# Kernel tuning notes

Measured on AMD Instinct MI355X. Metric: run time of the kernel, lower is better.

Reference implementation:

```python
import jax, jax.numpy as jnp
import numpy as np

EPS = 1e-8        # slot-attention epsilon
LN_EPS = 1e-5     # torch LayerNorm default
NUM_ITERS = 3

def _ln(x, g, b):
    m = jnp.mean(x, axis=-1, keepdims=True)
    v = jnp.var(x, axis=-1, keepdims=True)
    return (x - m) * jax.lax.rsqrt(v + LN_EPS) * g + b

def setup_inputs() -> dict:
    key = jax.random.key(0)
    ks = jax.random.split(key, 24)
    B, N, D, S, K, H = 64, 4096, 256, 256, 8, 512
    sc = 0.02
    return {
        "inputs": jax.random.normal(ks[0], (B, N, D), dtype=jnp.float32),
        "noise": jax.random.normal(ks[1], (B, K, S), dtype=jnp.float32),
        "slot_mu": jax.random.normal(ks[2], (1, 1, S)) * sc,
        "slot_log_sigma": jax.random.normal(ks[3], (1, 1, S)) * sc,
        "g_in": jnp.ones((D,)), "b_in": jnp.zeros((D,)),
        "g_sl": jnp.ones((S,)), "b_sl": jnp.zeros((S,)),
        "g_mlp": jnp.ones((S,)), "b_mlp": jnp.zeros((S,)),
        "Wq": jax.random.normal(ks[4], (S, S)) * sc,
        "Wk": jax.random.normal(ks[5], (S, D)) * sc,
        "Wv": jax.random.normal(ks[6], (S, D)) * sc,
        "W_ih": jax.random.normal(ks[7], (3 * S, S)) * sc,
        "W_hh": jax.random.normal(ks[8], (3 * S, S)) * sc,
        "b_ih": jnp.zeros((3 * S,)), "b_hh": jnp.zeros((3 * S,)),
        "W1": jax.random.normal(ks[9], (H, S)) * sc,
        "b1": jnp.zeros((H,)),
        "W2": jax.random.normal(ks[10], (S, H)) * sc,
        "b2": jnp.zeros((S,)),
    }

def _gru_cell(x, h, W_ih, W_hh, b_ih, b_hh):
    gi = x @ W_ih.T + b_ih
    gh = h @ W_hh.T + b_hh
    ir, iz, inn = jnp.split(gi, 3, axis=-1)
    hr, hz, hn = jnp.split(gh, 3, axis=-1)
    r = jax.nn.sigmoid(ir + hr)
    z = jax.nn.sigmoid(iz + hz)
    n = jnp.tanh(inn + r * hn)
    return (1.0 - z) * n + z * h

def reference(inputs, noise, slot_mu, slot_log_sigma, g_in, b_in, g_sl, b_sl,
              g_mlp, b_mlp, Wq, Wk, Wv, W_ih, W_hh, b_ih, b_hh, W1, b1, W2, b2):
    S = Wq.shape[0]
    slots = slot_mu + jnp.exp(slot_log_sigma) * noise          # [B,K,S]
    x = _ln(inputs, g_in, b_in)                                # [B,N,D]
    k = (x @ Wk.T) * (S ** -0.5)                               # [B,N,S]
    v = x @ Wv.T                                               # [B,N,S]
    for i in range(NUM_ITERS):
        slots_prev = slots
        q = _ln(slots, g_sl, b_sl) @ Wq.T                      # [B,K,S]
        attn_logits = jnp.einsum('bns,bks->bnk', k, q)         # [B,N,K]
        attn = jax.nn.softmax(attn_logits, axis=-1) + EPS      # softmax over slots
        attn = attn / jnp.sum(attn, axis=1, keepdims=True)     # normalize over inputs
        updates = jnp.einsum('bnk,bns->bks', attn, v)          # [B,K,S]
        slots = _gru_cell(updates, slots_prev, W_ih, W_hh, b_ih, b_hh)
        if i < NUM_ITERS - 1:
            h = jax.nn.relu(_ln(slots, g_mlp, b_mlp) @ W1.T + b1)
            slots = slots + (h @ W2.T + b2)
    return slots
```

## Files before the change

kernel.cpp:

```cpp
#include <hip/hip_runtime.h>
#include <math.h>

#define NB 64
#define NN 4096
#define ND 256
#define NS 256
#define NK 8
#define NH 512
#define NROW (NB*NN)
#define NSLOT (NB*NK)
#define EPSA 1e-8f

typedef unsigned short u16;
typedef unsigned int   u32;
typedef __bf16 bf16x8 __attribute__((ext_vector_type(8)));
typedef float  f32x4  __attribute__((ext_vector_type(4)));

__device__ __forceinline__ float bf2f(u16 u) {
  union { u32 i; float f; } v; v.i = ((u32)u) << 16; return v.f;
}
__device__ __forceinline__ u16 f2bf(float f) {
  union { float f; u32 i; } v; v.f = f;
  u32 x = v.i;
  return (u16)((x + 0x7FFFu + ((x >> 16) & 1u)) >> 16);
}

#define OFF_KV     0ULL
#define OFF_SLOTS  268435456ULL
#define OFF_QBF    268959744ULL
#define OFF_UPDP   269221888ULL
#define OFF_SUMSP  277610496ULL
#define OFF_WC     277643264ULL
#define OFF_WQT    277905408ULL
#define OFF_WIHT   278167552ULL
#define OFF_WHHT   278953984ULL
#define OFF_W1T    279740416ULL
#define OFF_W2T    280264704ULL

__global__ __launch_bounds__(256) void prep_kernel(
    const float* __restrict__ Wq, const float* __restrict__ Wk, const float* __restrict__ Wv,
    const float* __restrict__ Wih, const float* __restrict__ Whh,
    const float* __restrict__ W1, const float* __restrict__ W2,
    u16* __restrict__ Wc, float* __restrict__ WqT, float* __restrict__ WihT,
    float* __restrict__ WhhT, float* __restrict__ W1T, float* __restrict__ W2T)
{
  int idx = blockIdx.x * 256 + threadIdx.x;
  if (idx < 512*256) {
    int j = idx >> 8, d = idx & 255;
    float w = (j < 256) ? Wk[idx] * 0.0625f : Wv[idx - 65536];
    Wc[idx] = f2bf(w);
    W1T[d*512 + j] = W1[idx];
  }
  if (idx < 256*256) {
    int j = idx >> 8, d = idx & 255;
    WqT[d*256 + j] = Wq[idx];
  }
  if (idx < 768*256) {
    int j = idx >> 8, d = idx & 255;
    WihT[d*768 + j] = Wih[idx];
    WhhT[d*768 + j] = Whh[idx];
  }
  if (idx < 256*512) {
    int j = idx >> 9, h = idx & 511;
    W2T[h*256 + j] = W2[idx];
  }
}

__global__ __launch_bounds__(256) void slots_init_kernel(
    const float* __restrict__ noise, const float* __restrict__ mu,
    const float* __restrict__ lsig, float* __restrict__ slots)
{
  int idx = blockIdx.x * 256 + threadIdx.x;
  int s = idx & 255;
  slots[idx] = mu[s] + expf(lsig[s]) * noise[idx];
}

__global__ __launch_bounds__(256) void lngemm_kernel(
    const float* __restrict__ x, const float* __restrict__ gw, const float* __restrict__ bw,
    const u16* __restrict__ Wc, u16* __restrict__ kv)
{
  __shared__ u16 As[16384];
  __shared__ u16 Bs[16384];
  const int t = threadIdx.x, w = t >> 6, lane = t & 63;
  const int L15 = lane & 15, q4 = lane >> 4;
  const int blk = blockIdx.x;

  float4 gv = *(const float4*)(gw + lane*4);
  float4 bv = *(const float4*)(bw + lane*4);
  for (int i = 0; i < 16; ++i) {
    int m = w*16 + i;
    float4 xv = *(const float4*)(x + ((size_t)(blk*64 + m))*256 + lane*4);
    float s  = xv.x + xv.y + xv.z + xv.w;
    float sq = xv.x*xv.x + xv.y*xv.y + xv.z*xv.z + xv.w*xv.w;
    #pragma unroll
    for (int mm = 32; mm >= 1; mm >>= 1) { s += __shfl_xor(s, mm, 64); sq += __shfl_xor(sq, mm, 64); }
    float mean = s * (1.f/256.f);
    float rstd = rsqrtf(sq * (1.f/256.f) - mean*mean + 1e-5f);
    ushort4 o;
    o.x = f2bf((xv.x - mean)*rstd*gv.x + bv.x);
    o.y = f2bf((xv.y - mean)*rstd*gv.y + bv.y);
    o.z = f2bf((xv.z - mean)*rstd*gv.z + bv.z);
    o.w = f2bf((xv.w - mean)*rstd*gv.w + bv.w);
    int swz = (lane >> 1) ^ (m & 7);
    *(ushort4*)&As[m*256 + swz*8 + (lane & 1)*4] = o;
  }
  for (int nc = 0; nc < 8; ++nc) {
    #pragma unroll
    for (int i = 0; i < 8; ++i) {
      int slot = i*4 + w;
      int g = slot*64 + lane;
      int jr = g >> 5, c = g & 31;
      const u16* src = Wc + ((size_t)(nc*64 + jr))*256 + ((c ^ (jr & 7)) << 3);
      __builtin_amdgcn_global_load_lds(
        (const __attribute__((address_space(1))) u32*)src,
        (__attribute__((address_space(3))) u32*)((char*)Bs + slot*1024 + lane*16), 16, 0, 0);
    }
    __syncthreads();
    f32x4 acc[4] = {};
    #pragma unroll
    for (int ks = 0; ks < 8; ++ks) {
      int swz = (ks*4 + q4) ^ (L15 & 7);
      bf16x8 af = *(const bf16x8*)&As[(w*16 + L15)*256 + swz*8];
      #pragma unroll
      for (int nt = 0; nt < 4; ++nt) {
        bf16x8 bf = *(const bf16x8*)&Bs[(nt*16 + L15)*256 + swz*8];
        acc[nt] = __builtin_amdgcn_mfma_f32_16x16x32_bf16(af, bf, acc[nt], 0, 0, 0);
      }
    }
    __syncthreads();
    #pragma unroll
    for (int nt = 0; nt < 4; ++nt)
      #pragma unroll
      for (int reg = 0; reg < 4; ++reg) {
        size_t row = (size_t)blk*64 + w*16 + q4*4 + reg;
        int col = nc*64 + nt*16 + L15;
        kv[row*512 + col] = f2bf(acc[nt][reg]);
      }
  }
}

__global__ __launch_bounds__(256) void q_kernel(
    const float* __restrict__ slots, const float* __restrict__ gw, const float* __restrict__ bw,
    const float* __restrict__ WqT, u16* __restrict__ qbf)
{
  __shared__ float ln[2][256];
  int t = threadIdx.x, wv = t >> 6, lane = t & 63;
  int base = blockIdx.x * 2;
  if (wv < 2) {
    int row = base + wv;
    float4 xv = *(const float4*)(slots + (size_t)row*256 + lane*4);
    float s  = xv.x + xv.y + xv.z + xv.w;
    float sq = xv.x*xv.x + xv.y*xv.y + xv.z*xv.z + xv.w*xv.w;
    #pragma unroll
    for (int m = 32; m >= 1; m >>= 1) { s += __shfl_xor(s, m, 64); sq += __shfl_xor(sq, m, 64); }
    float mean = s * (1.f/256.f);
    float rstd = rsqrtf(sq * (1.f/256.f) - mean*mean + 1e-5f);
    float4 gv = *(const float4*)(gw + lane*4);
    float4 bv = *(const float4*)(bw + lane*4);
    ln[wv][lane*4+0] = (xv.x - mean)*rstd*gv.x + bv.x;
    ln[wv][lane*4+1] = (xv.y - mean)*rstd*gv.y + bv.y;
    ln[wv][lane*4+2] = (xv.z - mean)*rstd*gv.z + bv.z;
    ln[wv][lane*4+3] = (xv.w - mean)*rstd*gv.w + bv.w;
  }
  __syncthreads();
  float a0 = 0.f, a1 = 0.f;
  for (int d = 0; d < 256; ++d) {
    float w = WqT[d*256 + t];
    a0 += ln[0][d] * w;
    a1 += ln[1][d] * w;
  }
  qbf[(size_t)base*256 + t]     = f2bf(a0);
  qbf[(size_t)(base+1)*256 + t] = f2bf(a1);
}

__global__ __launch_bounds__(256) void attn_kernel(
    const u16* __restrict__ kv, const u16* __restrict__ qbf,
    float* __restrict__ updp, float* __restrict__ sums_p)
{
  __shared__ u16 tile[16384];
  __shared__ u16 attn_bf[16*72];
  __shared__ float sums_w[4][8];
  const int b = blockIdx.x, cg = blockIdx.y;
  const int t = threadIdx.x, w = t >> 6, lane = t & 63;
  const int L15 = lane & 15, q4 = lane >> 4;

  if (t < 32) sums_w[t >> 3][t & 7] = 0.f;

  bf16x8 qf[8];
  {
    int slot = (L15 < 8) ? L15 : 7;
    const u16* qp = qbf + ((size_t)b*8 + slot)*256;
    #pragma unroll
    for (int ks = 0; ks < 8; ++ks)
      qf[ks] = *(const bf16x8*)(qp + ks*32 + q4*8);
  }

  f32x4 accp[4] = {};
  for (int cc = 0; cc < 4; ++cc) {
    const int n0 = cg*256 + cc*64;
    uint4 vr[8];
    #pragma unroll
    for (int j = 0; j < 8; ++j) {
      int idx = j*256 + t;
      int n = idx >> 5, dc = idx & 31;
      vr[j] = *(const uint4*)(kv + ((size_t)(b*4096 + n0 + n))*512 + 256 + dc*8);
    }
    #pragma unroll
    for (int i = 0; i < 8; ++i) {
      int slot = i*4 + w;
      int g = slot*64 + lane;
      int lr = g >> 5, c = g & 31;
      const u16* src = kv + ((size_t)(b*4096 + n0 + lr))*512 + ((c ^ (lr & 7)) << 3);
      __builtin_amdgcn_global_load_lds(
        (const __attribute__((address_space(1))) u32*)src,
        (__attribute__((address_space(3))) u32*)((char*)tile + slot*1024 + lane*16), 16, 0, 0);
    }
    __syncthreads();
    f32x4 lg = {};
    #pragma unroll
    for (int ks = 0; ks < 8; ++ks) {
      int swz = (ks*4 + q4) ^ (L15 & 7);
      bf16x8 af = *(const bf16x8*)&tile[(w*16 + L15)*256 + swz*8];
      lg = __builtin_amdgcn_mfma_f32_16x16x32_bf16(af, qf[ks], lg, 0, 0, 0);
    }
    float attnv[4], tot = 0.f;
    #pragma unroll
    for (int reg = 0; reg < 4; ++reg) {
      float val = lg[reg];
      float mx = val;
      mx = fmaxf(mx, __shfl_xor(mx, 1, 64));
      mx = fmaxf(mx, __shfl_xor(mx, 2, 64));
      mx = fmaxf(mx, __shfl_xor(mx, 4, 64));
      float e = expf(val - mx);
      float se = e;
      se += __shfl_xor(se, 1, 64);
      se += __shfl_xor(se, 2, 64);
      se += __shfl_xor(se, 4, 64);
      attnv[reg] = e / se + EPSA;
      tot += attnv[reg];
    }
    tot += __shfl_xor(tot, 16, 64);
    tot += __shfl_xor(tot, 32, 64);
    __syncthreads();
    #pragma unroll
    for (int j = 0; j < 8; ++j) {
      int idx = j*256 + t;
      int n = idx >> 5, dc = idx & 31;
      u32 words[4] = {vr[j].x, vr[j].y, vr[j].z, vr[j].w};
      #pragma unroll
      for (int e = 0; e < 8; ++e) {
        int d = dc*8 + e;
        int f = (dc + e) & 7;
        int swz = (n >> 3) ^ f;
        tile[d*64 + swz*8 + (n & 7)] = (u16)(words[e >> 1] >> ((e & 1)*16));
      }
    }
    if (L15 < 8) {
      #pragma unroll
      for (int reg = 0; reg < 4; ++reg)
        attn_bf[L15*72 + w*16 + q4*4 + reg] = f2bf(attnv[reg]);
      if (lane < 8) sums_w[w][lane] += tot;
    }
    __syncthreads();
    #pragma unroll
    for (int ks = 0; ks < 2; ++ks) {
      bf16x8 paf = *(const bf16x8*)&attn_bf[L15*72 + ks*32 + q4*8];
      #pragma unroll
      for (int nt = 0; nt < 4; ++nt) {
        int d = (w*4 + nt)*16 + L15;
        int swz = (ks*4 + q4) ^ ((d + (d >> 3)) & 7);
        bf16x8 vbf = *(const bf16x8*)&tile[d*64 + swz*8];
        accp[nt] = __builtin_amdgcn_mfma_f32_16x16x32_bf16(paf, vbf, accp[nt], 0, 0, 0);
      }
    }
    __syncthreads();
  }
  float* up = updp + ((size_t)(b*16 + cg))*2048;
  if (q4 < 2) {
    #pragma unroll
    for (int nt = 0; nt < 4; ++nt) {
      int d = (w*4 + nt)*16 + L15;
      #pragma unroll
      for (int reg = 0; reg < 4; ++reg)
        up[(q4*4 + reg)*256 + d] = accp[nt][reg];
    }
  }
  if (t < 8)
    sums_p[(b*16 + cg)*8 + t] = sums_w[0][t] + sums_w[1][t] + sums_w[2][t] + sums_w[3][t];
}

__global__ __launch_bounds__(256) void grumlp_kernel(
    const float* __restrict__ updp, const float* __restrict__ sums_p,
    const float* __restrict__ WihT, const float* __restrict__ WhhT,
    const float* __restrict__ bih, const float* __restrict__ bhh,
    const float* __restrict__ gm, const float* __restrict__ bm,
    const float* __restrict__ W1T, const float* __restrict__ b1,
    const float* __restrict__ W2T, const float* __restrict__ b2,
    float* __restrict__ slots, int do_mlp)
{
  __shared__ float xs[4][256], hs[4][256];
  __shared__ float ln[4][256];
  __shared__ float hb[4][512];
  int t = threadIdx.x, w = t >> 6, lane = t & 63;
  int base = blockIdx.x * 4;
  #pragma unroll
  for (int g = 0; g < 4; ++g) {
    int row = base + g;
    int b = row >> 3, s = row & 7;
    float u = 0.f, sm = 0.f;
    for (int c = 0; c < 16; ++c) {
      u  += updp[((size_t)(b*16 + c)*8 + s)*256 + t];
      sm += sums_p[(b*16 + c)*8 + s];
    }
    xs[g][t] = u / sm;
    hs[g][t] = slots[(size_t)row*256 + t];
  }
  __syncthreads();
  float ra[4] = {}, za[4] = {}, ia[4] = {}, ha[4] = {};
  for (int d = 0; d < 256; ++d) {
    float wir = WihT[d*768 + t], wiz = WihT[d*768 + 256 + t], win = WihT[d*768 + 512 + t];
    float whr = WhhT[d*768 + t], whz = WhhT[d*768 + 256 + t], whn = WhhT[d*768 + 512 + t];
    #pragma unroll
    for (int g = 0; g < 4; ++g) {
      float xx = xs[g][d], hh = hs[g][d];
      ra[g] += xx*wir + hh*whr;
      za[g] += xx*wiz + hh*whz;
      ia[g] += xx*win;
      ha[g] += hh*whn;
    }
  }
  float bir = bih[t], biz = bih[256+t], bin = bih[512+t];
  float bhr = bhh[t], bhz = bhh[256+t], bhn = bhh[512+t];
  float nv[4];
  #pragma unroll
  for (int g = 0; g < 4; ++g) {
    float r  = 1.f/(1.f + expf(-(ra[g] + bir + bhr)));
    float z  = 1.f/(1.f + expf(-(za[g] + biz + bhz)));
    float nn = tanhf(ia[g] + bin + r*(ha[g] + bhn));
    nv[g] = (1.f - z)*nn + z*hs[g][t];
  }
  if (!do_mlp) {
    #pragma unroll
    for (int g = 0; g < 4; ++g)
      slots[(size_t)(base+g)*256 + t] = nv[g];
    return;
  }
  #pragma unroll
  for (int g = 0; g < 4; ++g) xs[g][t] = nv[g];
  __syncthreads();
  {
    float4 xv = *(const float4*)&xs[w][lane*4];
    float s  = xv.x + xv.y + xv.z + xv.w;
    float sq = xv.x*xv.x + xv.y*xv.y + xv.z*xv.z + xv.w*xv.w;
    #pragma unroll
    for (int m = 32; m >= 1; m >>= 1) { s += __shfl_xor(s, m, 64); sq += __shfl_xor(sq, m, 64); }
    float mean = s * (1.f/256.f);
    float rstd = rsqrtf(sq * (1.f/256.f) - mean*mean + 1e-5f);
    float4 gv = *(const float4*)(gm + lane*4);
    float4 bv = *(const float4*)(bm + lane*4);
    ln[w][lane*4+0] = (xv.x - mean)*rstd*gv.x + bv.x;
    ln[w][lane*4+1] = (xv.y - mean)*rstd*gv.y + bv.y;
    ln[w][lane*4+2] = (xv.z - mean)*rstd*gv.z + bv.z;
    ln[w][lane*4+3] = (xv.w - mean)*rstd*gv.w + bv.w;
  }
  __syncthreads();
  float h0[4] = {}, h1[4] = {};
  for (int d = 0; d < 256; ++d) {
    float w0 = W1T[d*512 + t], w1 = W1T[d*512 + 256 + t];
    #pragma unroll
    for (int g = 0; g < 4; ++g) { float l = ln[g][d]; h0[g] += l*w0; h1[g] += l*w1; }
  }
  float bb0 = b1[t], bb1 = b1[256 + t];
  #pragma unroll
  for (int g = 0; g < 4; ++g) {
    hb[g][t]       = fmaxf(h0[g] + bb0, 0.f);
    hb[g][256 + t] = fmaxf(h1[g] + bb1, 0.f);
  }
  __syncthreads();
  float o[4] = {};
  for (int hh = 0; hh < 512; ++hh) {
    float ww = W2T[hh*256 + t];
    #pragma unroll
    for (int g = 0; g < 4; ++g) o[g] += hb[g][hh] * ww;
  }
  float b2v = b2[t];
  #pragma unroll
  for (int g = 0; g < 4; ++g)
    slots[(size_t)(base+g)*256 + t] = xs[g][t] + o[g] + b2v;
}

extern "C" void kernel_launch(void* const* d_in, const int* in_sizes, int n_in,
                              void* d_out, int out_size, void* d_ws, size_t ws_size,
                              hipStream_t stream)
{
  (void)in_sizes; (void)n_in; (void)out_size; (void)ws_size;
  const float* inputs = (const float*)d_in[0];
  const float* noise  = (const float*)d_in[1];
  const float* mu     = (const float*)d_in[2];
  const float* lsig   = (const float*)d_in[3];
  const float* g_in   = (const float*)d_in[4];
  const float* b_in   = (const float*)d_in[5];
  const float* g_sl   = (const float*)d_in[6];
  const float* b_sl   = (const float*)d_in[7];
  const float* g_mlp  = (const float*)d_in[8];
  const float* b_mlp  = (const float*)d_in[9];
  const float* Wq     = (const float*)d_in[10];
  const float* Wk     = (const float*)d_in[11];
  const float* Wv     = (const float*)d_in[12];
  const float* Wih    = (const float*)d_in[13];
  const float* Whh    = (const float*)d_in[14];
  const float* bih    = (const float*)d_in[15];
  const float* bhh    = (const float*)d_in[16];
  const float* W1     = (const float*)d_in[17];
  const float* b1     = (const float*)d_in[18];
  const float* W2     = (const float*)d_in[19];
  const float* b2     = (const float*)d_in[20];

  char* ws = (char*)d_ws;
  u16*   kv     = (u16*)  (ws + OFF_KV);
  float* slots  = (float*)(ws + OFF_SLOTS);
  u16*   qb     = (u16*)  (ws + OFF_QBF);
  float* updp   = (float*)(ws + OFF_UPDP);
  float* sums_p = (float*)(ws + OFF_SUMSP);
  u16*   Wc     = (u16*)  (ws + OFF_WC);
  float* WqT    = (float*)(ws + OFF_WQT);
  float* WihT   = (float*)(ws + OFF_WIHT);
  float* WhhT   = (float*)(ws + OFF_WHHT);
  float* W1T    = (float*)(ws + OFF_W1T);
  float* W2T    = (float*)(ws + OFF_W2T);

  prep_kernel<<<768, 256, 0, stream>>>(Wq, Wk, Wv, Wih, Whh, W1, W2,
                                       Wc, WqT, WihT, WhhT, W1T, W2T);
  slots_init_kernel<<<512, 256, 0, stream>>>(noise, mu, lsig, slots);
  lngemm_kernel<<<NROW/64, 256, 0, stream>>>(inputs, g_in, b_in, Wc, kv);

  for (int it = 0; it < 3; ++it) {
    q_kernel<<<NSLOT/2, 256, 0, stream>>>(slots, g_sl, b_sl, WqT, qb);
    attn_kernel<<<dim3(NB, 16), 256, 0, stream>>>(kv, qb, updp, sums_p);
    grumlp_kernel<<<NSLOT/4, 256, 0, stream>>>(updp, sums_p, WihT, WhhT, bih, bhh,
                                               g_mlp, b_mlp, W1T, b1, W2T, b2,
                                               slots, (it < 2) ? 1 : 0);
  }
  hipMemcpyAsync(d_out, slots, (size_t)NSLOT*NS*sizeof(float),
                 hipMemcpyDeviceToDevice, stream);
}
```

Baseline: 1.038 ms.

## Split K and transposed V into separate buffers and simplify attention kernel

The LN+projection GEMM now writes K row-major and V transposed (d-major per batch) into separate buffers, reading weights directly from global memory with a 64x64 register tile per wave and a smaller shared buffer. The attention kernel drops its per-chunk LDS staging and in-register V transpose. It reads K and V^T fragments straight from global memory, and the grid doubles to 32 chunk groups of 128 rows. This removes repeated shuffle and transpose work in each of the three iterations, at the cost of a transposed store pass in the one-time GEMM and twice as many partial results to reduce in the GRU kernel.

```diff
diff --git a/kernel.cpp b/kernel.cpp
--- a/kernel.cpp
+++ b/kernel.cpp
@@ -10,6 +10,7 @@
 #define NROW (NB*NN)
 #define NSLOT (NB*NK)
 #define EPSA 1e-8f
+#define NCG 32
 
 typedef unsigned short u16;
 typedef unsigned int   u32;
@@ -25,17 +26,18 @@
   return (u16)((x + 0x7FFFu + ((x >> 16) & 1u)) >> 16);
 }
 
-#define OFF_KV     0ULL
+#define OFF_KG     0ULL
+#define OFF_VTG    134217728ULL
 #define OFF_SLOTS  268435456ULL
 #define OFF_QBF    268959744ULL
 #define OFF_UPDP   269221888ULL
-#define OFF_SUMSP  277610496ULL
-#define OFF_WC     277643264ULL
-#define OFF_WQT    277905408ULL
-#define OFF_WIHT   278167552ULL
-#define OFF_WHHT   278953984ULL
-#define OFF_W1T    279740416ULL
-#define OFF_W2T    280264704ULL
+#define OFF_SUMSP  285999104ULL
+#define OFF_WC     286064640ULL
+#define OFF_WQT    286326784ULL
+#define OFF_WIHT   286588928ULL
+#define OFF_WHHT   287375360ULL
+#define OFF_W1T    288161792ULL
+#define OFF_W2T    288686080ULL
 
 __global__ __launch_bounds__(256) void prep_kernel(
     const float* __restrict__ Wq, const float* __restrict__ Wk, const float* __restrict__ Wv,
@@ -75,67 +77,115 @@
   slots[idx] = mu[s] + expf(lsig[s]) * noise[idx];
 }
 
-__global__ __launch_bounds__(256) void lngemm_kernel(
+__global__ __launch_bounds__(256, 4) void lngemm_kernel(
     const float* __restrict__ x, const float* __restrict__ gw, const float* __restrict__ bw,
-    const u16* __restrict__ Wc, u16* __restrict__ kv)
-{
-  __shared__ u16 As[16384];
-  __shared__ u16 Bs[16384];
+    const u16* __restrict__ Wc, u16* __restrict__ kg, u16* __restrict__ vtg)
+{
+  __shared__ u16 sh[16384];
   const int t = threadIdx.x, w = t >> 6, lane = t & 63;
   const int L15 = lane & 15, q4 = lane >> 4;
   const int blk = blockIdx.x;
 
   float4 gv = *(const float4*)(gw + lane*4);
   float4 bv = *(const float4*)(bw + lane*4);
-  for (int i = 0; i < 16; ++i) {
-    int m = w*16 + i;
-    float4 xv = *(const float4*)(x + ((size_t)(blk*64 + m))*256 + lane*4);
-    float s  = xv.x + xv.y + xv.z + xv.w;
-    float sq = xv.x*xv.x + xv.y*xv.y + xv.z*xv.z + xv.w*xv.w;
-    #pragma unroll
-    for (int mm = 32; mm >= 1; mm >>= 1) { s += __shfl_xor(s, mm, 64); sq += __shfl_xor(sq, mm, 64); }
-    float mean = s * (1.f/256.f);
-    float rstd = rsqrtf(sq * (1.f/256.f) - mean*mean + 1e-5f);
-    ushort4 o;
-    o.x = f2bf((xv.x - mean)*rstd*gv.x + bv.x);
-    o.y = f2bf((xv.y - mean)*rstd*gv.y + bv.y);
-    o.z = f2bf((xv.z - mean)*rstd*gv.z + bv.z);
-    o.w = f2bf((xv.w - mean)*rstd*gv.w + bv.w);
-    int swz = (lane >> 1) ^ (m & 7);
-    *(ushort4*)&As[m*256 + swz*8 + (lane & 1)*4] = o;
-  }
-  for (int nc = 0; nc < 8; ++nc) {
+  #pragma unroll
+  for (int grp = 0; grp < 2; ++grp) {
+    float4 xv[8]; float s[8], sq[8];
     #pragma unroll
     for (int i = 0; i < 8; ++i) {
-      int slot = i*4 + w;
-      int g = slot*64 + lane;
-      int jr = g >> 5, c = g & 31;
-      const u16* src = Wc + ((size_t)(nc*64 + jr))*256 + ((c ^ (jr & 7)) << 3);
-      __builtin_amdgcn_global_load_lds(
-        (const __attribute__((address_space(1))) u32*)src,
-        (__attribute__((address_space(3))) u32*)((char*)Bs + slot*1024 + lane*16), 16, 0, 0);
-    }
-    __syncthreads();
-    f32x4 acc[4] = {};
-    #pragma unroll
+      int m = w*16 + grp*8 + i;
+      xv[i] = *(const float4*)(x + ((size_t)(blk*64 + m))*256 + lane*4);
+    }
+    #pragma unroll
+    for (int i = 0; i < 8; ++i) {
+      s[i]  = xv[i].x + xv[i].y + xv[i].z + xv[i].w;
+      sq[i] = xv[i].x*xv[i].x + xv[i].y*xv[i].y + xv[i].z*xv[i].z + xv[i].w*xv[i].w;
+    }
+    #pragma unroll
+    for (int mm = 32; mm >= 1; mm >>= 1)
+      #pragma unroll
+      for (int i = 0; i < 8; ++i) {
+        s[i]  += __shfl_xor(s[i],  mm, 64);
+        sq[i] += __shfl_xor(sq[i], mm, 64);
+      }
+    #pragma unroll
+    for (int i = 0; i < 8; ++i) {
+      int m = w*16 + grp*8 + i;
+      float mean = s[i] * (1.f/256.f);
+      float rstd = rsqrtf(sq[i] * (1.f/256.f) - mean*mean + 1e-5f);
+      ushort4 o;
+      o.x = f2bf((xv[i].x - mean)*rstd*gv.x + bv.x);
+      o.y = f2bf((xv[i].y - mean)*rstd*gv.y + bv.y);
+      o.z = f2bf((xv[i].z - mean)*rstd*gv.z + bv.z);
+      o.w = f2bf((xv[i].w - mean)*rstd*gv.w + bv.w);
+      int swz = (lane >> 1) ^ (m & 7);
+      *(ushort4*)&sh[m*256 + swz*8 + (lane & 1)*4] = o;
+    }
+  }
+  __syncthreads();
+
+  f32x4 acc[4][4];
+  #pragma unroll
+  for (int p = 0; p < 2; ++p) {
+    #pragma unroll
+    for (int j = 0; j < 4; ++j)
+      #pragma unroll
+      for (int mt = 0; mt < 4; ++mt)
+        acc[j][mt] = (f32x4){0.f, 0.f, 0.f, 0.f};
     for (int ks = 0; ks < 8; ++ks) {
-      int swz = (ks*4 + q4) ^ (L15 & 7);
-      bf16x8 af = *(const bf16x8*)&As[(w*16 + L15)*256 + swz*8];
-      #pragma unroll
-      for (int nt = 0; nt < 4; ++nt) {
-        bf16x8 bf = *(const bf16x8*)&Bs[(nt*16 + L15)*256 + swz*8];
-        acc[nt] = __builtin_amdgcn_mfma_f32_16x16x32_bf16(af, bf, acc[nt], 0, 0, 0);
+      bf16x8 bf[4], af[4];
+      #pragma unroll
+      for (int j = 0; j < 4; ++j) {
+        int col = (p*16 + j*4 + w)*16 + L15;
+        bf[j] = *(const bf16x8*)(Wc + (size_t)col*256 + ks*32 + q4*8);
       }
-    }
-    __syncthreads();
-    #pragma unroll
-    for (int nt = 0; nt < 4; ++nt)
-      #pragma unroll
-      for (int reg = 0; reg < 4; ++reg) {
-        size_t row = (size_t)blk*64 + w*16 + q4*4 + reg;
-        int col = nc*64 + nt*16 + L15;
-        kv[row*512 + col] = f2bf(acc[nt][reg]);
+      #pragma unroll
+      for (int mt = 0; mt < 4; ++mt)
+        af[mt] = *(const bf16x8*)&sh[(mt*16 + L15)*256 + (((ks*4 + q4) ^ (L15 & 7)) << 3)];
+      #pragma unroll
+      for (int j = 0; j < 4; ++j)
+        #pragma unroll
+        for (int mt = 0; mt < 4; ++mt)
+          acc[j][mt] = __builtin_amdgcn_mfma_f32_16x16x32_bf16(af[mt], bf[j], acc[j][mt], 0, 0, 0);
+    }
+    if (p == 0) {
+      #pragma unroll
+      for (int j = 0; j < 4; ++j) {
+        int col = (j*4 + w)*16 + L15;
+        #pragma unroll
+        for (int mt = 0; mt < 4; ++mt)
+          #pragma unroll
+          for (int r = 0; r < 4; ++r) {
+            size_t row = (size_t)blk*64 + mt*16 + q4*4 + r;
+            kg[row*256 + col] = f2bf(acc[j][mt][r]);
+          }
       }
+    }
+  }
+  __syncthreads();
+  #pragma unroll
+  for (int j = 0; j < 4; ++j) {
+    int d = (j*4 + w)*16 + L15;
+    #pragma unroll
+    for (int mt = 0; mt < 4; ++mt) {
+      int c = mt*2 + (q4 >> 1);
+      u32 lo = (u32)f2bf(acc[j][mt][0]) | ((u32)f2bf(acc[j][mt][1]) << 16);
+      u32 hi = (u32)f2bf(acc[j][mt][2]) | ((u32)f2bf(acc[j][mt][3]) << 16);
+      u32* p32 = (u32*)&sh[d*64 + ((c ^ (d & 7)) << 3) + (q4 & 1)*4];
+      p32[0] = lo; p32[1] = hi;
+    }
+  }
+  __syncthreads();
+  {
+    int bb = blk >> 6;
+    int nbase = (blk & 63)*64;
+    #pragma unroll
+    for (int i = 0; i < 8; ++i) {
+      int d = i*32 + w*8 + (lane >> 3);
+      int c = lane & 7;
+      uint4 vv = *(const uint4*)&sh[d*64 + ((c ^ (d & 7)) << 3)];
+      *(uint4*)(vtg + (size_t)bb*1048576 + (size_t)d*4096 + nbase + c*8) = vv;
+    }
   }
 }
 
@@ -173,60 +223,43 @@
   qbf[(size_t)(base+1)*256 + t] = f2bf(a1);
 }
 
-__global__ __launch_bounds__(256) void attn_kernel(
-    const u16* __restrict__ kv, const u16* __restrict__ qbf,
+__global__ __launch_bounds__(256, 4) void attn_kernel(
+    const u16* __restrict__ kg, const u16* __restrict__ vtg, const u16* __restrict__ qbf,
     float* __restrict__ updp, float* __restrict__ sums_p)
 {
-  __shared__ u16 tile[16384];
-  __shared__ u16 attn_bf[16*72];
+  __shared__ u16 attnT[8*128];
   __shared__ float sums_w[4][8];
   const int b = blockIdx.x, cg = blockIdx.y;
   const int t = threadIdx.x, w = t >> 6, lane = t & 63;
   const int L15 = lane & 15, q4 = lane >> 4;
-
-  if (t < 32) sums_w[t >> 3][t & 7] = 0.f;
+  const int n0 = cg*128;
+  const int slot = L15 & 7;
 
   bf16x8 qf[8];
   {
-    int slot = (L15 < 8) ? L15 : 7;
     const u16* qp = qbf + ((size_t)b*8 + slot)*256;
     #pragma unroll
     for (int ks = 0; ks < 8; ++ks)
       qf[ks] = *(const bf16x8*)(qp + ks*32 + q4*8);
   }
 
-  f32x4 accp[4] = {};
-  for (int cc = 0; cc < 4; ++cc) {
-    const int n0 = cg*256 + cc*64;
-    uint4 vr[8];
-    #pragma unroll
-    for (int j = 0; j < 8; ++j) {
-      int idx = j*256 + t;
-      int n = idx >> 5, dc = idx & 31;
-      vr[j] = *(const uint4*)(kv + ((size_t)(b*4096 + n0 + n))*512 + 256 + dc*8);
-    }
-    #pragma unroll
-    for (int i = 0; i < 8; ++i) {
-      int slot = i*4 + w;
-      int g = slot*64 + lane;
-      int lr = g >> 5, c = g & 31;
-      const u16* src = kv + ((size_t)(b*4096 + n0 + lr))*512 + ((c ^ (lr & 7)) << 3);
-      __builtin_amdgcn_global_load_lds(
-        (const __attribute__((address_space(1))) u32*)src,
-        (__attribute__((address_space(3))) u32*)((char*)tile + slot*1024 + lane*16), 16, 0, 0);
-    }
-    __syncthreads();
-    f32x4 lg = {};
+  f32x4 lg[2] = {};
+  #pragma unroll
+  for (int mt = 0; mt < 2; ++mt) {
+    const u16* krow = kg + ((size_t)(b*4096 + n0 + mt*64 + w*16 + L15))*256;
     #pragma unroll
     for (int ks = 0; ks < 8; ++ks) {
-      int swz = (ks*4 + q4) ^ (L15 & 7);
-      bf16x8 af = *(const bf16x8*)&tile[(w*16 + L15)*256 + swz*8];
-      lg = __builtin_amdgcn_mfma_f32_16x16x32_bf16(af, qf[ks], lg, 0, 0, 0);
-    }
-    float attnv[4], tot = 0.f;
-    #pragma unroll
-    for (int reg = 0; reg < 4; ++reg) {
-      float val = lg[reg];
+      bf16x8 af = *(const bf16x8*)(krow + ks*32 + q4*8);
+      lg[mt] = __builtin_amdgcn_mfma_f32_16x16x32_bf16(af, qf[ks], lg[mt], 0, 0, 0);
+    }
+  }
+  float tot = 0.f;
+  #pragma unroll
+  for (int mt = 0; mt < 2; ++mt) {
+    float av[4];
+    #pragma unroll
+    for (int r = 0; r < 4; ++r) {
+      float val = lg[mt][r];
       float mx = val;
       mx = fmaxf(mx, __shfl_xor(mx, 1, 64));
       mx = fmaxf(mx, __shfl_xor(mx, 2, 64));
@@ -236,57 +269,45 @@
       se += __shfl_xor(se, 1, 64);
       se += __shfl_xor(se, 2, 64);
       se += __shfl_xor(se, 4, 64);
-      attnv[reg] = e / se + EPSA;
-      tot += attnv[reg];
-    }
-    tot += __shfl_xor(tot, 16, 64);
-    tot += __shfl_xor(tot, 32, 64);
-    __syncthreads();
-    #pragma unroll
-    for (int j = 0; j < 8; ++j) {
-      int idx = j*256 + t;
-      int n = idx >> 5, dc = idx & 31;
-      u32 words[4] = {vr[j].x, vr[j].y, vr[j].z, vr[j].w};
-      #pragma unroll
-      for (int e = 0; e < 8; ++e) {
-        int d = dc*8 + e;
-        int f = (dc + e) & 7;
-        int swz = (n >> 3) ^ f;
-        tile[d*64 + swz*8 + (n & 7)] = (u16)(words[e >> 1] >> ((e & 1)*16));
-      }
+      av[r] = e / se + EPSA;
+      tot += av[r];
     }
     if (L15 < 8) {
-      #pragma unroll
-      for (int reg = 0; reg < 4; ++reg)
-        attn_bf[L15*72 + w*16 + q4*4 + reg] = f2bf(attnv[reg]);
-      if (lane < 8) sums_w[w][lane] += tot;
-    }
-    __syncthreads();
-    #pragma unroll
-    for (int ks = 0; ks < 2; ++ks) {
-      bf16x8 paf = *(const bf16x8*)&attn_bf[L15*72 + ks*32 + q4*8];
-      #pragma unroll
-      for (int nt = 0; nt < 4; ++nt) {
-        int d = (w*4 + nt)*16 + L15;
-        int swz = (ks*4 + q4) ^ ((d + (d >> 3)) & 7);
-        bf16x8 vbf = *(const bf16x8*)&tile[d*64 + swz*8];
-        accp[nt] = __builtin_amdgcn_mfma_f32_16x16x32_bf16(paf, vbf, accp[nt], 0, 0, 0);
-      }
-    }
-    __syncthreads();
-  }
-  float* up = updp + ((size_t)(b*16 + cg))*2048;
+      int c = mt*8 + w*2 + (q4 >> 1);
+      u32 lo = (u32)f2bf(av[0]) | ((u32)f2bf(av[1]) << 16);
+      u32 hi = (u32)f2bf(av[2]) | ((u32)f2bf(av[3]) << 16);
+      u32* p32 = (u32*)&attnT[slot*128 + ((c ^ (slot*2)) << 3) + (q4 & 1)*4];
+      p32[0] = lo; p32[1] = hi;
+    }
+  }
+  tot += __shfl_xor(tot, 16, 64);
+  tot += __shfl_xor(tot, 32, 64);
+  if (q4 == 0 && L15 < 8) sums_w[w][L15] = tot;
+  __syncthreads();
+
+  f32x4 accp[4] = {};
+  for (int ks = 0; ks < 4; ++ks) {
+    int c = ks*4 + q4;
+    bf16x8 pa = *(const bf16x8*)&attnT[slot*128 + ((c ^ (slot*2)) << 3)];
+    #pragma unroll
+    for (int nt = 0; nt < 4; ++nt) {
+      int d = (nt*4 + w)*16 + L15;
+      bf16x8 vb = *(const bf16x8*)(vtg + (size_t)b*1048576 + (size_t)d*4096 + n0 + ks*32 + q4*8);
+      accp[nt] = __builtin_amdgcn_mfma_f32_16x16x32_bf16(pa, vb, accp[nt], 0, 0, 0);
+    }
+  }
   if (q4 < 2) {
+    float* up = updp + ((size_t)(b*NCG + cg))*2048;
     #pragma unroll
     for (int nt = 0; nt < 4; ++nt) {
-      int d = (w*4 + nt)*16 + L15;
-      #pragma unroll
-      for (int reg = 0; reg < 4; ++reg)
-        up[(q4*4 + reg)*256 + d] = accp[nt][reg];
+      int d = (nt*4 + w)*16 + L15;
+      #pragma unroll
+      for (int r = 0; r < 4; ++r)
+        up[(q4*4 + r)*256 + d] = accp[nt][r];
     }
   }
   if (t < 8)
-    sums_p[(b*16 + cg)*8 + t] = sums_w[0][t] + sums_w[1][t] + sums_w[2][t] + sums_w[3][t];
+    sums_p[(b*NCG + cg)*8 + t] = sums_w[0][t] + sums_w[1][t] + sums_w[2][t] + sums_w[3][t];
 }
 
 __global__ __launch_bounds__(256) void grumlp_kernel(
@@ -308,9 +329,9 @@
     int row = base + g;
     int b = row >> 3, s = row & 7;
     float u = 0.f, sm = 0.f;
-    for (int c = 0; c < 16; ++c) {
-      u  += updp[((size_t)(b*16 + c)*8 + s)*256 + t];
-      sm += sums_p[(b*16 + c)*8 + s];
+    for (int c = 0; c < NCG; ++c) {
+      u  += updp[((size_t)(b*NCG + c)*8 + s)*256 + t];
+      sm += sums_p[(b*NCG + c)*8 + s];
     }
     xs[g][t] = u / sm;
     hs[g][t] = slots[(size_t)row*256 + t];
@@ -417,7 +438,8 @@
   const float* b2     = (const float*)d_in[20];
 
   char* ws = (char*)d_ws;
-  u16*   kv     = (u16*)  (ws + OFF_KV);
+  u16*   kg     = (u16*)  (ws + OFF_KG);
+  u16*   vtg    = (u16*)  (ws + OFF_VTG);
   float* slots  = (float*)(ws + OFF_SLOTS);
   u16*   qb     = (u16*)  (ws + OFF_QBF);
   float* updp   = (float*)(ws + OFF_UPDP);
@@ -432,11 +454,11 @@
   prep_kernel<<<768, 256, 0, stream>>>(Wq, Wk, Wv, Wih, Whh, W1, W2,
                                        Wc, WqT, WihT, WhhT, W1T, W2T);
   slots_init_kernel<<<512, 256, 0, stream>>>(noise, mu, lsig, slots);
-  lngemm_kernel<<<NROW/64, 256, 0, stream>>>(inputs, g_in, b_in, Wc, kv);
+  lngemm_kernel<<<NROW/64, 256, 0, stream>>>(inputs, g_in, b_in, Wc, kg, vtg);
 
   for (int it = 0; it < 3; ++it) {
     q_kernel<<<NSLOT/2, 256, 0, stream>>>(slots, g_sl, b_sl, WqT, qb);
-    attn_kernel<<<dim3(NB, 16), 256, 0, stream>>>(kv, qb, updp, sums_p);
+    attn_kernel<<<dim3(NB, NCG), 256, 0, stream>>>(kg, vtg, qb, updp, sums_p);
     grumlp_kernel<<<NSLOT/4, 256, 0, stream>>>(updp, sums_p, WihT, WhhT, bih, bhh,
                                                g_mlp, b_mlp, W1T, b1, W2T, b2,
                                                slots, (it < 2) ? 1 : 0);
```

Measured after the change: 1.106 ms. 6.6% more time.
